# Kernel tuning notes

Hardware: AMD Instinct MI355X
Metric: run time of the kernel (lower is better)

The kernel has to match this reference:

```python
import jax, jax.numpy as jnp
import numpy as np

N = 50000          # nodes
E = 600000         # edges (before self-loops)
IN = 256           # input feature dim
HID = 64           # hidden channels per head
HEADS = 4          # attention heads (hidden layers)
OUT = 64           # output channels (last layer, heads=1)
NEG_SLOPE = 0.2    # PyG GATConv default leaky-relu slope


def setup_inputs() -> dict:
    key = jax.random.key(0)
    ks = jax.random.split(key, 16)
    s = 0.05
    x = jax.random.normal(ks[0], (N, IN), jnp.float32)
    edge_index = jax.random.randint(ks[1], (2, E), 0, N, jnp.int32)
    # layer 0: IN -> HEADS*HID
    W0 = jax.random.normal(ks[2], (IN, HEADS * HID), jnp.float32) * s
    a0s = jax.random.normal(ks[3], (HEADS, HID), jnp.float32) * s
    a0d = jax.random.normal(ks[4], (HEADS, HID), jnp.float32) * s
    b0 = jnp.zeros((HEADS * HID,), jnp.float32)
    # layer 1: HEADS*HID -> HEADS*HID
    W1 = jax.random.normal(ks[5], (HEADS * HID, HEADS * HID), jnp.float32) * s
    a1s = jax.random.normal(ks[6], (HEADS, HID), jnp.float32) * s
    a1d = jax.random.normal(ks[7], (HEADS, HID), jnp.float32) * s
    b1 = jnp.zeros((HEADS * HID,), jnp.float32)
    # layer 2 (output): HEADS*HID -> OUT, heads=1
    W2 = jax.random.normal(ks[8], (HEADS * HID, OUT), jnp.float32) * s
    a2s = jax.random.normal(ks[9], (1, OUT), jnp.float32) * s
    a2d = jax.random.normal(ks[10], (1, OUT), jnp.float32) * s
    b2 = jnp.zeros((OUT,), jnp.float32)
    return dict(x=x, edge_index=edge_index,
                W0=W0, a0s=a0s, a0d=a0d, b0=b0,
                W1=W1, a1s=a1s, a1d=a1d, b1=b1,
                W2=W2, a2s=a2s, a2d=a2d, b2=b2)


def _gat_conv(x, src, dst, deg, W, a_s, a_d, b, heads, out_ch):
    """PyG-style GATConv with self-loops already in (src, dst); mean aggregation."""
    n = x.shape[0]
    h = (x @ W).reshape(n, heads, out_ch)                 # [N, H, C]
    alpha_s = jnp.sum(h * a_s, axis=-1)                   # [N, H]
    alpha_d = jnp.sum(h * a_d, axis=-1)                   # [N, H]
    e = jax.nn.leaky_relu(alpha_s[src] + alpha_d[dst], NEG_SLOPE)  # [Etot, H]
    # segment softmax over incoming edges of each dst node
    m = jax.ops.segment_max(e, dst, num_segments=n)       # [N, H]
    ex = jnp.exp(e - m[dst])
    denom = jax.ops.segment_sum(ex, dst, num_segments=n)  # [N, H]
    alpha = ex / denom[dst]                               # [Etot, H]
    msg = h[src] * alpha[..., None]                       # [Etot, H, C]
    out = jax.ops.segment_sum(msg, dst, num_segments=n)   # [N, H, C]
    out = out / deg[:, None, None]                        # aggr='mean'
    return out.reshape(n, heads * out_ch) + b


def reference(x, edge_index, W0, a0s, a0d, b0, W1, a1s, a1d, b1, W2, a2s, a2d, b2):
    n = x.shape[0]
    # PyG GATConv adds self-loops by default; edge_index constant across layers
    loop = jnp.arange(n, dtype=edge_index.dtype)
    src = jnp.concatenate([edge_index[0], loop])
    dst = jnp.concatenate([edge_index[1], loop])
    deg = jax.ops.segment_sum(jnp.ones(src.shape[0], jnp.float32), dst, num_segments=n)
    h = _gat_conv(x, src, dst, deg, W0, a0s, a0d, b0, HEADS, HID)
    h = jax.nn.relu(h)   # dropout is identity at inference
    h = _gat_conv(h, src, dst, deg, W1, a1s, a1d, b1, HEADS, HID)
    h = jax.nn.relu(h)
    out = _gat_conv(h, src, dst, deg, W2, a2s, a2d, b2, 1, OUT)
    return out
```

## Files before the change

kernel.cpp:

```cpp
#include <hip/hip_runtime.h>
#include <hip/hip_fp16.h>

#define NEG_SLOPE 0.2f

typedef _Float16 f16x8 __attribute__((ext_vector_type(8)));
typedef _Float16 f16x4 __attribute__((ext_vector_type(4)));
typedef float f32x4 __attribute__((ext_vector_type(4)));

__global__ void zero_int_kernel(int* __restrict__ p, int n) {
  int i = blockIdx.x * blockDim.x + threadIdx.x;
  if (i < n) p[i] = 0;
}

__global__ void zero2_float_kernel(float* __restrict__ p1, float* __restrict__ p2,
                                   int n) {
  int i = blockIdx.x * blockDim.x + threadIdx.x;
  if (i < n) { p1[i] = 0.f; p2[i] = 0.f; }
}

__global__ void count_kernel(const int* __restrict__ ei, int E, int N,
                             int* __restrict__ cnt) {
  int e = blockIdx.x * blockDim.x + threadIdx.x;
  int tot = E + N;
  if (e >= tot) return;
  int dst = (e < E) ? ei[E + e] : (e - E);
  atomicAdd(&cnt[dst], 1);
}

__global__ __launch_bounds__(256) void scanA_kernel(const int* __restrict__ cnt,
                                                    int* __restrict__ locex,
                                                    int* __restrict__ blk_sum,
                                                    int N) {
  int t = threadIdx.x;
  int base = blockIdx.x * 1024 + t * 4;
  int a0 = 0, a1 = 0, a2 = 0, a3 = 0;
  if (base + 3 < N) {
    int4 v = *(const int4*)&cnt[base];
    a0 = v.x; a1 = v.y; a2 = v.z; a3 = v.w;
  } else if (base < N) {
    a0 = cnt[base];
    if (base + 1 < N) a1 = cnt[base + 1];
    if (base + 2 < N) a2 = cnt[base + 2];
  }
  int s1 = a0 + a1, s2 = s1 + a2, s3 = s2 + a3;
  int tot = s3;
  int lane = t & 63, wid = t >> 6;
  int ws = tot;
#pragma unroll
  for (int off = 1; off < 64; off <<= 1) {
    int u = __shfl_up(ws, off, 64);
    if (lane >= off) ws += u;
  }
  __shared__ int wsum[4];
  __shared__ int woff[4];
  if (lane == 63) wsum[wid] = ws;
  __syncthreads();
  if (t == 0) {
    int r = 0;
#pragma unroll
    for (int i = 0; i < 4; ++i) { woff[i] = r; r += wsum[i]; }
    blk_sum[blockIdx.x] = r;
  }
  __syncthreads();
  int ex = woff[wid] + (ws - tot);
  int o0 = ex, o1 = ex + a0, o2 = ex + s1, o3 = ex + s2;
  if (base + 3 < N) {
    *(int4*)&locex[base] = make_int4(o0, o1, o2, o3);
  } else if (base < N) {
    locex[base] = o0;
    if (base + 1 < N) locex[base + 1] = o1;
    if (base + 2 < N) locex[base + 2] = o2;
  }
}

__global__ void scanB_kernel(const int* __restrict__ blk_sum,
                             int* __restrict__ blk_off,
                             int* __restrict__ row_ptr, int nb, int N) {
  int t = threadIdx.x;
  int run = 0;
  for (int c = 0; c < nb; c += 64) {
    int idx = c + t;
    int v = (idx < nb) ? blk_sum[idx] : 0;
    int inc = v;
#pragma unroll
    for (int off = 1; off < 64; off <<= 1) {
      int u = __shfl_up(inc, off, 64);
      if (t >= off) inc += u;
    }
    if (idx < nb) blk_off[idx] = run + inc - v;
    run += __shfl(inc, 63, 64);
  }
  if (t == 0) row_ptr[N] = run;
}

__global__ void scanC_kernel(const int* __restrict__ locex,
                             const int* __restrict__ blk_off,
                             int* __restrict__ row_ptr,
                             int* __restrict__ cursor, int N) {
  int i = blockIdx.x * blockDim.x + threadIdx.x;
  if (i >= N) return;
  int v = blk_off[i >> 10] + locex[i];
  row_ptr[i] = v;
  cursor[i] = v;
}

__global__ void fill_kernel(const int* __restrict__ ei, int E, int N,
                            int* __restrict__ cursor, int* __restrict__ col_src) {
  int e = blockIdx.x * blockDim.x + threadIdx.x;
  int tot = E + N;
  if (e >= tot) return;
  int src, dst;
  if (e < E) { src = ei[e]; dst = ei[E + e]; } else { src = e - E; dst = e - E; }
  int pos = atomicAdd(&cursor[dst], 1);
  col_src[pos] = src;
}

template <int BN, int H>
__global__ __launch_bounds__(256) void mfma_gemm(const float* __restrict__ X,
                                                 const float* __restrict__ W,
                                                 __half* __restrict__ Y16,
                                                 const float* __restrict__ aS,
                                                 const float* __restrict__ aD,
                                                 float* __restrict__ as_out,
                                                 float* __restrict__ ad_out,
                                                 int M, int N, int K) {
  constexpr int BM = 128, BK = 32;
  constexpr int LDK = BK + 8;
  constexpr int MI = (BN == 128) ? 4 : 2;
  constexpr int NI = 4;
  constexpr int CK = BN / 8;
  __shared__ _Float16 Ah[BM][LDK];
  __shared__ _Float16 Al[BM][LDK];
  __shared__ _Float16 Bh[BN][LDK];
  __shared__ _Float16 Bl[BN][LDK];
  int tid = threadIdx.x;
  int wave = tid >> 6, lane = tid & 63;
  int quad = lane >> 4, l16 = lane & 15;
  int br = blockIdx.y * BM, bc = blockIdx.x * BN;
  int wm = (BN == 128) ? (wave >> 1) * 64 : wave * 32;
  int wn = (BN == 128) ? (wave & 1) * 64 : 0;
  int bn = tid % BN;
  int bkh = (tid / BN) * CK;

  f32x4 acc[MI][NI] = {};

  for (int k0 = 0; k0 < K; k0 += BK) {
#pragma unroll
    for (int i = 0; i < 4; ++i) {
      int f = tid + i * 256;
      int row = f >> 3;
      int kq = (f & 7) * 4;
      int gm = br + row;
      float4 v = make_float4(0.f, 0.f, 0.f, 0.f);
      if (gm < M) v = *(const float4*)&X[(size_t)gm * K + k0 + kq];
      f16x4 hi, lo;
      hi[0] = (_Float16)v.x; lo[0] = (_Float16)(v.x - (float)hi[0]);
      hi[1] = (_Float16)v.y; lo[1] = (_Float16)(v.y - (float)hi[1]);
      hi[2] = (_Float16)v.z; lo[2] = (_Float16)(v.z - (float)hi[2]);
      hi[3] = (_Float16)v.w; lo[3] = (_Float16)(v.w - (float)hi[3]);
      *(f16x4*)&Ah[row][kq] = hi;
      *(f16x4*)&Al[row][kq] = lo;
    }
    {
      float tmp[CK];
#pragma unroll
      for (int i = 0; i < CK; ++i)
        tmp[i] = W[(size_t)(k0 + bkh + i) * N + bc + bn];
#pragma unroll
      for (int c = 0; c < CK / 8; ++c) {
        f16x8 hi8, lo8;
#pragma unroll
        for (int j = 0; j < 8; ++j) {
          float v = tmp[c * 8 + j];
          _Float16 h = (_Float16)v;
          hi8[j] = h;
          lo8[j] = (_Float16)(v - (float)h);
        }
        *(f16x8*)&Bh[bn][bkh + c * 8] = hi8;
        *(f16x8*)&Bl[bn][bkh + c * 8] = lo8;
      }
    }
    __syncthreads();
    f16x8 fah[MI], fal[MI], fbh[NI], fbl[NI];
#pragma unroll
    for (int mi = 0; mi < MI; ++mi) {
      int row = wm + mi * 16 + l16;
      fah[mi] = *(const f16x8*)&Ah[row][quad * 8];
      fal[mi] = *(const f16x8*)&Al[row][quad * 8];
    }
#pragma unroll
    for (int ni = 0; ni < NI; ++ni) {
      int col = wn + ni * 16 + l16;
      fbh[ni] = *(const f16x8*)&Bh[col][quad * 8];
      fbl[ni] = *(const f16x8*)&Bl[col][quad * 8];
    }
#pragma unroll
    for (int mi = 0; mi < MI; ++mi)
#pragma unroll
      for (int ni = 0; ni < NI; ++ni) {
        acc[mi][ni] = __builtin_amdgcn_mfma_f32_16x16x32_f16(
            fah[mi], fbh[ni], acc[mi][ni], 0, 0, 0);
        acc[mi][ni] = __builtin_amdgcn_mfma_f32_16x16x32_f16(
            fah[mi], fbl[ni], acc[mi][ni], 0, 0, 0);
        acc[mi][ni] = __builtin_amdgcn_mfma_f32_16x16x32_f16(
            fal[mi], fbh[ni], acc[mi][ni], 0, 0, 0);
      }
    __syncthreads();
  }

#pragma unroll
  for (int mi = 0; mi < MI; ++mi) {
#pragma unroll
    for (int r = 0; r < 4; ++r) {
      int grow = br + wm + mi * 16 + quad * 4 + r;
      if (grow >= M) continue;
#pragma unroll
      for (int ni = 0; ni < NI; ++ni) {
        int gcol = bc + wn + ni * 16 + l16;
        Y16[(size_t)grow * N + gcol] = __float2half(acc[mi][ni][r]);
      }
    }
  }

  int head = (bc + wn) >> 6;
  float as_v[NI], ad_v[NI];
#pragma unroll
  for (int ni = 0; ni < NI; ++ni) {
    int c = (wn + ni * 16 + l16) & 63;
    as_v[ni] = aS[head * 64 + c];
    ad_v[ni] = aD[head * 64 + c];
  }
#pragma unroll
  for (int mi = 0; mi < MI; ++mi) {
#pragma unroll
    for (int r = 0; r < 4; ++r) {
      float s = 0.f, d = 0.f;
#pragma unroll
      for (int ni = 0; ni < NI; ++ni) {
        s += acc[mi][ni][r] * as_v[ni];
        d += acc[mi][ni][r] * ad_v[ni];
      }
      s += __shfl_xor(s, 1, 64); d += __shfl_xor(d, 1, 64);
      s += __shfl_xor(s, 2, 64); d += __shfl_xor(d, 2, 64);
      s += __shfl_xor(s, 4, 64); d += __shfl_xor(d, 4, 64);
      s += __shfl_xor(s, 8, 64); d += __shfl_xor(d, 8, 64);
      if (l16 == 0) {
        int grow = br + wm + mi * 16 + quad * 4 + r;
        if (grow < M) {
          atomicAdd(&as_out[(size_t)grow * H + head], s);
          atomicAdd(&ad_out[(size_t)grow * H + head], d);
        }
      }
    }
  }
}

__device__ __forceinline__ void fma_h4(const __half* p, float w, float* facc) {
  union { float2 f2; __half2 h2[2]; } c;
  c.f2 = *(const float2*)p;
  float2 lo = __half22float2(c.h2[0]);
  float2 hi = __half22float2(c.h2[1]);
  facc[0] += lo.x * w; facc[1] += lo.y * w;
  facc[2] += hi.x * w; facc[3] += hi.y * w;
}

template <bool RELU>
__global__ void aggregate4_kernel(const __half* __restrict__ h16,
                                  const float* __restrict__ as_,
                                  const float* __restrict__ ad_,
                                  const int* __restrict__ row_ptr,
                                  const int* __restrict__ col_src,
                                  const float* __restrict__ bias,
                                  float* __restrict__ out, int N) {
  int lane = threadIdx.x & 63;
  int node = (blockIdx.x * blockDim.x + threadIdx.x) >> 6;
  if (node >= N) return;
  int beg = row_ptr[node], end = row_ptr[node + 1];
  int deg = end - beg;
  float inv_deg = 1.f / (float)deg;
  int myhead = lane >> 4;
  float facc[4] = {};
  float4 adv4 = *(const float4*)(ad_ + (size_t)node * 4);
  const __half* hl = h16 + lane * 4;

  if (deg <= 16) {
    int head_w = lane >> 4, e_w = lane & 15;
    float q = 0.f; int s_w = 0;
    if (e_w < deg) {
      s_w = col_src[beg + e_w];
      float4 a4 = *(const float4*)(as_ + (size_t)s_w * 4);
      float av = head_w == 0 ? a4.x : head_w == 1 ? a4.y : head_w == 2 ? a4.z : a4.w;
      float dv = head_w == 0 ? adv4.x : head_w == 1 ? adv4.y : head_w == 2 ? adv4.z : adv4.w;
      float e = av + dv;
      e = (e > 0.f) ? e : NEG_SLOPE * e;
      q = __expf(e);
    }
    float dn = q;
    dn += __shfl_xor(dn, 1, 64);
    dn += __shfl_xor(dn, 2, 64);
    dn += __shfl_xor(dn, 4, 64);
    dn += __shfl_xor(dn, 8, 64);
    float qs = q * (1.f / dn) * inv_deg;
    int base = myhead << 4;
    int i = 0;
    for (; i + 4 <= deg; i += 4) {
      int s0 = __shfl(s_w, base + i + 0, 64); float w0 = __shfl(qs, base + i + 0, 64);
      int s1 = __shfl(s_w, base + i + 1, 64); float w1 = __shfl(qs, base + i + 1, 64);
      int s2 = __shfl(s_w, base + i + 2, 64); float w2 = __shfl(qs, base + i + 2, 64);
      int s3 = __shfl(s_w, base + i + 3, 64); float w3 = __shfl(qs, base + i + 3, 64);
      fma_h4(hl + (size_t)s0 * 256, w0, facc);
      fma_h4(hl + (size_t)s1 * 256, w1, facc);
      fma_h4(hl + (size_t)s2 * 256, w2, facc);
      fma_h4(hl + (size_t)s3 * 256, w3, facc);
    }
    for (; i < deg; ++i) {
      int srcn = __shfl(s_w, base + i, 64);
      float w = __shfl(qs, base + i, 64);
      fma_h4(hl + (size_t)srcn * 256, w, facc);
    }
  } else if (deg <= 64) {
    float p0 = 0.f, p1 = 0.f, p2 = 0.f, p3 = 0.f; int s_w = 0;
    if (lane < deg) {
      s_w = col_src[beg + lane];
      float4 a4 = *(const float4*)(as_ + (size_t)s_w * 4);
      float e0 = a4.x + adv4.x; e0 = e0 > 0.f ? e0 : NEG_SLOPE * e0; p0 = __expf(e0);
      float e1 = a4.y + adv4.y; e1 = e1 > 0.f ? e1 : NEG_SLOPE * e1; p1 = __expf(e1);
      float e2 = a4.z + adv4.z; e2 = e2 > 0.f ? e2 : NEG_SLOPE * e2; p2 = __expf(e2);
      float e3 = a4.w + adv4.w; e3 = e3 > 0.f ? e3 : NEG_SLOPE * e3; p3 = __expf(e3);
    }
    float d0 = p0, d1 = p1, d2 = p2, d3 = p3;
#pragma unroll
    for (int off = 32; off >= 1; off >>= 1) {
      d0 += __shfl_xor(d0, off, 64);
      d1 += __shfl_xor(d1, off, 64);
      d2 += __shfl_xor(d2, off, 64);
      d3 += __shfl_xor(d3, off, 64);
    }
    p0 *= (1.f / d0) * inv_deg;
    p1 *= (1.f / d1) * inv_deg;
    p2 *= (1.f / d2) * inv_deg;
    p3 *= (1.f / d3) * inv_deg;
    int i = 0;
    for (; i + 2 <= deg; i += 2) {
      int s0 = __shfl(s_w, i + 0, 64);
      int s1 = __shfl(s_w, i + 1, 64);
      float a00 = __shfl(p0, i + 0, 64), a01 = __shfl(p1, i + 0, 64);
      float a02 = __shfl(p2, i + 0, 64), a03 = __shfl(p3, i + 0, 64);
      float a10 = __shfl(p0, i + 1, 64), a11 = __shfl(p1, i + 1, 64);
      float a12 = __shfl(p2, i + 1, 64), a13 = __shfl(p3, i + 1, 64);
      float w0 = myhead == 0 ? a00 : myhead == 1 ? a01 : myhead == 2 ? a02 : a03;
      float w1 = myhead == 0 ? a10 : myhead == 1 ? a11 : myhead == 2 ? a12 : a13;
      fma_h4(hl + (size_t)s0 * 256, w0, facc);
      fma_h4(hl + (size_t)s1 * 256, w1, facc);
    }
    for (; i < deg; ++i) {
      int srcn = __shfl(s_w, i, 64);
      float b0 = __shfl(p0, i, 64), b1 = __shfl(p1, i, 64);
      float b2 = __shfl(p2, i, 64), b3 = __shfl(p3, i, 64);
      float w = myhead == 0 ? b0 : myhead == 1 ? b1 : myhead == 2 ? b2 : b3;
      fma_h4(hl + (size_t)srcn * 256, w, facc);
    }
  } else {
    float dn0 = 0.f, dn1 = 0.f, dn2 = 0.f, dn3 = 0.f;
    for (int i = beg + lane; i < end; i += 64) {
      int s = col_src[i];
      float4 a4 = *(const float4*)(as_ + (size_t)s * 4);
      float e0 = a4.x + adv4.x; e0 = e0 > 0.f ? e0 : NEG_SLOPE * e0; dn0 += __expf(e0);
      float e1 = a4.y + adv4.y; e1 = e1 > 0.f ? e1 : NEG_SLOPE * e1; dn1 += __expf(e1);
      float e2 = a4.z + adv4.z; e2 = e2 > 0.f ? e2 : NEG_SLOPE * e2; dn2 += __expf(e2);
      float e3 = a4.w + adv4.w; e3 = e3 > 0.f ? e3 : NEG_SLOPE * e3; dn3 += __expf(e3);
    }
#pragma unroll
    for (int off = 32; off >= 1; off >>= 1) {
      dn0 += __shfl_xor(dn0, off, 64);
      dn1 += __shfl_xor(dn1, off, 64);
      dn2 += __shfl_xor(dn2, off, 64);
      dn3 += __shfl_xor(dn3, off, 64);
    }
    float adm = myhead == 0 ? adv4.x : myhead == 1 ? adv4.y : myhead == 2 ? adv4.z : adv4.w;
    float invdn = 1.f / (myhead == 0 ? dn0 : myhead == 1 ? dn1 : myhead == 2 ? dn2 : dn3);
    invdn *= inv_deg;
    for (int i = beg; i < end; ++i) {
      int s = col_src[i];
      float e = as_[(size_t)s * 4 + myhead] + adm;
      e = (e > 0.f) ? e : NEG_SLOPE * e;
      float w = __expf(e) * invdn;
      fma_h4(hl + (size_t)s * 256, w, facc);
    }
  }

  float* orow = out + (size_t)node * 256 + lane * 4;
#pragma unroll
  for (int p = 0; p < 4; ++p) {
    float v = facc[p] + bias[lane * 4 + p];
    if (RELU) v = fmaxf(v, 0.f);
    orow[p] = v;
  }
}

template <bool RELU>
__global__ void aggregate1_kernel(const __half* __restrict__ h16,
                                  const float* __restrict__ as_,
                                  const float* __restrict__ ad_,
                                  const int* __restrict__ row_ptr,
                                  const int* __restrict__ col_src,
                                  const float* __restrict__ bias,
                                  float* __restrict__ out, int N) {
  int lane = threadIdx.x & 63;
  int node = (blockIdx.x * blockDim.x + threadIdx.x) >> 6;
  if (node >= N) return;
  int beg = row_ptr[node], end = row_ptr[node + 1];
  int deg = end - beg;
  float inv_deg = 1.f / (float)deg;
  float adv = ad_[node];
  const __half* hb = h16 + lane;
  float facc = 0.f;

  if (deg <= 64) {
    float q = 0.f; int s_w = 0;
    if (lane < deg) {
      s_w = col_src[beg + lane];
      float e = as_[s_w] + adv;
      e = (e > 0.f) ? e : NEG_SLOPE * e;
      q = __expf(e);
    }
    float dn = q;
#pragma unroll
    for (int off = 32; off >= 1; off >>= 1) dn += __shfl_xor(dn, off, 64);
    float qs = q * (1.f / dn) * inv_deg;
    int deg8 = (deg + 7) & ~7;
    for (int i = 0; i < deg8; i += 8) {
      int s0 = __shfl(s_w, i + 0, 64); float w0 = __shfl(qs, i + 0, 64);
      int s1 = __shfl(s_w, i + 1, 64); float w1 = __shfl(qs, i + 1, 64);
      int s2 = __shfl(s_w, i + 2, 64); float w2 = __shfl(qs, i + 2, 64);
      int s3 = __shfl(s_w, i + 3, 64); float w3 = __shfl(qs, i + 3, 64);
      int s4 = __shfl(s_w, i + 4, 64); float w4 = __shfl(qs, i + 4, 64);
      int s5 = __shfl(s_w, i + 5, 64); float w5 = __shfl(qs, i + 5, 64);
      int s6 = __shfl(s_w, i + 6, 64); float w6 = __shfl(qs, i + 6, 64);
      int s7 = __shfl(s_w, i + 7, 64); float w7 = __shfl(qs, i + 7, 64);
      float v0 = __half2float(hb[(size_t)s0 * 64]);
      float v1 = __half2float(hb[(size_t)s1 * 64]);
      float v2 = __half2float(hb[(size_t)s2 * 64]);
      float v3 = __half2float(hb[(size_t)s3 * 64]);
      float v4 = __half2float(hb[(size_t)s4 * 64]);
      float v5 = __half2float(hb[(size_t)s5 * 64]);
      float v6 = __half2float(hb[(size_t)s6 * 64]);
      float v7 = __half2float(hb[(size_t)s7 * 64]);
      facc += v0 * w0 + v1 * w1 + v2 * w2 + v3 * w3;
      facc += v4 * w4 + v5 * w5 + v6 * w6 + v7 * w7;
    }
  } else {
    float dn = 0.f;
    for (int i = beg + lane; i < end; i += 64) {
      int s = col_src[i];
      float e = as_[s] + adv;
      e = (e > 0.f) ? e : NEG_SLOPE * e;
      dn += __expf(e);
    }
#pragma unroll
    for (int off = 32; off >= 1; off >>= 1) dn += __shfl_xor(dn, off, 64);
    float scale = (1.f / dn) * inv_deg;
    for (int base = beg; base < end; base += 64) {
      int i2 = base + lane;
      float q2 = 0.f; int s2r = 0;
      if (i2 < end) {
        s2r = col_src[i2];
        float e = as_[s2r] + adv;
        e = (e > 0.f) ? e : NEG_SLOPE * e;
        q2 = __expf(e) * scale;
      }
      int cnt = end - base; if (cnt > 64) cnt = 64;
      for (int j = 0; j < cnt; ++j) {
        int s = __shfl(s2r, j, 64);
        float w = __shfl(q2, j, 64);
        facc += __half2float(hb[(size_t)s * 64]) * w;
      }
    }
  }

  float vout = facc + bias[lane];
  if (RELU) vout = fmaxf(vout, 0.f);
  out[(size_t)node * 64 + lane] = vout;
}

extern "C" void kernel_launch(void* const* d_in, const int* in_sizes, int n_in,
                              void* d_out, int out_size, void* d_ws, size_t ws_size,
                              hipStream_t stream) {
  const float* x   = (const float*)d_in[0];
  const int*   ei  = (const int*)d_in[1];
  const float* W0  = (const float*)d_in[2];
  const float* a0s = (const float*)d_in[3];
  const float* a0d = (const float*)d_in[4];
  const float* b0  = (const float*)d_in[5];
  const float* W1  = (const float*)d_in[6];
  const float* a1s = (const float*)d_in[7];
  const float* a1d = (const float*)d_in[8];
  const float* b1  = (const float*)d_in[9];
  const float* W2  = (const float*)d_in[10];
  const float* a2s = (const float*)d_in[11];
  const float* a2d = (const float*)d_in[12];
  const float* b2  = (const float*)d_in[13];

  const int IN = 256;
  const int N = in_sizes[0] / IN;
  const int E = in_sizes[1] / 2;
  const int Etot = E + N;
  const int nb = (N + 1023) / 1024;

  char* ws = (char*)d_ws;
  size_t off = 0;
  auto alloc = [&](size_t bytes) {
    void* p = ws + off;
    off += (bytes + 255) & ~(size_t)255;
    return p;
  };
  float*  Bbuf    = (float*)alloc((size_t)N * 256 * 4);
  __half* A16     = (__half*)alloc((size_t)N * 256 * 2);
  float*  as_buf  = (float*)alloc((size_t)N * 4 * 4);
  float*  ad_buf  = (float*)alloc((size_t)N * 4 * 4);
  int*    row_ptr = (int*)alloc((size_t)(N + 1) * 4);
  int*    cursor  = (int*)alloc((size_t)N * 4);
  int*    cnt     = (int*)alloc((size_t)N * 4);
  int*    col_src = (int*)alloc((size_t)Etot * 4);
  int*    locex   = (int*)alloc((size_t)N * 4);
  int*    blk_sum = (int*)alloc((size_t)nb * 4);
  int*    blk_off = (int*)alloc((size_t)nb * 4);

  zero_int_kernel<<<(N + 255) / 256, 256, 0, stream>>>(cnt, N);
  count_kernel<<<(Etot + 255) / 256, 256, 0, stream>>>(ei, E, N, cnt);
  scanA_kernel<<<nb, 256, 0, stream>>>(cnt, locex, blk_sum, N);
  scanB_kernel<<<1, 64, 0, stream>>>(blk_sum, blk_off, row_ptr, nb, N);
  scanC_kernel<<<(N + 255) / 256, 256, 0, stream>>>(locex, blk_off, row_ptr, cursor, N);
  fill_kernel<<<(Etot + 255) / 256, 256, 0, stream>>>(ei, E, N, cursor, col_src);

  dim3 g0(256 / 128, (N + 127) / 128);
  dim3 g2(64 / 64, (N + 127) / 128);
  int node_blocks = (N + 3) / 4;
  int zblk4 = (N * 4 + 255) / 256;
  int zblk1 = (N + 255) / 256;

  zero2_float_kernel<<<zblk4, 256, 0, stream>>>(as_buf, ad_buf, N * 4);
  mfma_gemm<128, 4><<<g0, 256, 0, stream>>>(x, W0, A16, a0s, a0d,
                                            as_buf, ad_buf, N, 256, 256);
  aggregate4_kernel<true><<<node_blocks, 256, 0, stream>>>(
      A16, as_buf, ad_buf, row_ptr, col_src, b0, Bbuf, N);

  zero2_float_kernel<<<zblk4, 256, 0, stream>>>(as_buf, ad_buf, N * 4);
  mfma_gemm<128, 4><<<g0, 256, 0, stream>>>(Bbuf, W1, A16, a1s, a1d,
                                            as_buf, ad_buf, N, 256, 256);
  aggregate4_kernel<true><<<node_blocks, 256, 0, stream>>>(
      A16, as_buf, ad_buf, row_ptr, col_src, b1, Bbuf, N);

  zero2_float_kernel<<<zblk1, 256, 0, stream>>>(as_buf, ad_buf, N);
  mfma_gemm<64, 1><<<g2, 256, 0, stream>>>(Bbuf, W2, A16, a2s, a2d,
                                           as_buf, ad_buf, N, 64, 256);
  aggregate1_kernel<false><<<node_blocks, 256, 0, stream>>>(
      A16, as_buf, ad_buf, row_ptr, col_src, b2, (float*)d_out, N);
}
```

Before: 468.4 us.

## Pre-split weights to fp16 and load GEMM fragments directly from global memory

New measurement: 470.5 us. No clear change (+0.5%).

```diff
diff --git a/kernel.cpp b/kernel.cpp
--- a/kernel.cpp
+++ b/kernel.cpp
@@ -4,18 +4,11 @@
 #define NEG_SLOPE 0.2f
 
 typedef _Float16 f16x8 __attribute__((ext_vector_type(8)));
-typedef _Float16 f16x4 __attribute__((ext_vector_type(4)));
 typedef float f32x4 __attribute__((ext_vector_type(4)));
 
 __global__ void zero_int_kernel(int* __restrict__ p, int n) {
   int i = blockIdx.x * blockDim.x + threadIdx.x;
   if (i < n) p[i] = 0;
-}
-
-__global__ void zero2_float_kernel(float* __restrict__ p1, float* __restrict__ p2,
-                                   int n) {
-  int i = blockIdx.x * blockDim.x + threadIdx.x;
-  if (i < n) { p1[i] = 0.f; p2[i] = 0.f; }
 }
 
 __global__ void count_kernel(const int* __restrict__ ei, int E, int N,
@@ -115,84 +108,79 @@
   col_src[pos] = src;
 }
 
-template <int BN, int H>
+__global__ void wsplit_kernel(const float* __restrict__ W,
+                              _Float16* __restrict__ Wth,
+                              _Float16* __restrict__ Wtl, int K, int N) {
+  int idx = blockIdx.x * blockDim.x + threadIdx.x;
+  if (idx >= K * N) return;
+  int n = idx / K, k = idx - n * K;
+  float v = W[(size_t)k * N + n];
+  _Float16 h = (_Float16)v;
+  Wth[idx] = h;
+  Wtl[idx] = (_Float16)(v - (float)h);
+}
+
+template <int BN, int H, int K>
 __global__ __launch_bounds__(256) void mfma_gemm(const float* __restrict__ X,
-                                                 const float* __restrict__ W,
+                                                 const _Float16* __restrict__ Wth,
+                                                 const _Float16* __restrict__ Wtl,
                                                  __half* __restrict__ Y16,
                                                  const float* __restrict__ aS,
                                                  const float* __restrict__ aD,
                                                  float* __restrict__ as_out,
                                                  float* __restrict__ ad_out,
-                                                 int M, int N, int K) {
+                                                 int M, int N) {
   constexpr int BM = 128, BK = 32;
-  constexpr int LDK = BK + 8;
   constexpr int MI = (BN == 128) ? 4 : 2;
   constexpr int NI = 4;
-  constexpr int CK = BN / 8;
-  __shared__ _Float16 Ah[BM][LDK];
-  __shared__ _Float16 Al[BM][LDK];
-  __shared__ _Float16 Bh[BN][LDK];
-  __shared__ _Float16 Bl[BN][LDK];
   int tid = threadIdx.x;
   int wave = tid >> 6, lane = tid & 63;
   int quad = lane >> 4, l16 = lane & 15;
   int br = blockIdx.y * BM, bc = blockIdx.x * BN;
   int wm = (BN == 128) ? (wave >> 1) * 64 : wave * 32;
   int wn = (BN == 128) ? (wave & 1) * 64 : 0;
-  int bn = tid % BN;
-  int bkh = (tid / BN) * CK;
 
   f32x4 acc[MI][NI] = {};
 
+  const float* aptr[MI];
+  bool aval[MI];
+#pragma unroll
+  for (int mi = 0; mi < MI; ++mi) {
+    int grow = br + wm + mi * 16 + l16;
+    aval[mi] = grow < M;
+    aptr[mi] = X + (size_t)(aval[mi] ? grow : 0) * K + quad * 8;
+  }
+  const _Float16* bhp[NI];
+  const _Float16* blp[NI];
+#pragma unroll
+  for (int ni = 0; ni < NI; ++ni) {
+    int col = bc + wn + ni * 16 + l16;
+    bhp[ni] = Wth + (size_t)col * K + quad * 8;
+    blp[ni] = Wtl + (size_t)col * K + quad * 8;
+  }
+
+#pragma unroll 2
   for (int k0 = 0; k0 < K; k0 += BK) {
-#pragma unroll
-    for (int i = 0; i < 4; ++i) {
-      int f = tid + i * 256;
-      int row = f >> 3;
-      int kq = (f & 7) * 4;
-      int gm = br + row;
-      float4 v = make_float4(0.f, 0.f, 0.f, 0.f);
-      if (gm < M) v = *(const float4*)&X[(size_t)gm * K + k0 + kq];
-      f16x4 hi, lo;
-      hi[0] = (_Float16)v.x; lo[0] = (_Float16)(v.x - (float)hi[0]);
-      hi[1] = (_Float16)v.y; lo[1] = (_Float16)(v.y - (float)hi[1]);
-      hi[2] = (_Float16)v.z; lo[2] = (_Float16)(v.z - (float)hi[2]);
-      hi[3] = (_Float16)v.w; lo[3] = (_Float16)(v.w - (float)hi[3]);
-      *(f16x4*)&Ah[row][kq] = hi;
-      *(f16x4*)&Al[row][kq] = lo;
-    }
-    {
-      float tmp[CK];
-#pragma unroll
-      for (int i = 0; i < CK; ++i)
-        tmp[i] = W[(size_t)(k0 + bkh + i) * N + bc + bn];
-#pragma unroll
-      for (int c = 0; c < CK / 8; ++c) {
-        f16x8 hi8, lo8;
-#pragma unroll
-        for (int j = 0; j < 8; ++j) {
-          float v = tmp[c * 8 + j];
-          _Float16 h = (_Float16)v;
-          hi8[j] = h;
-          lo8[j] = (_Float16)(v - (float)h);
-        }
-        *(f16x8*)&Bh[bn][bkh + c * 8] = hi8;
-        *(f16x8*)&Bl[bn][bkh + c * 8] = lo8;
-      }
-    }
-    __syncthreads();
     f16x8 fah[MI], fal[MI], fbh[NI], fbl[NI];
 #pragma unroll
+    for (int ni = 0; ni < NI; ++ni) {
+      fbh[ni] = *(const f16x8*)(bhp[ni] + k0);
+      fbl[ni] = *(const f16x8*)(blp[ni] + k0);
+    }
+#pragma unroll
     for (int mi = 0; mi < MI; ++mi) {
-      int row = wm + mi * 16 + l16;
-      fah[mi] = *(const f16x8*)&Ah[row][quad * 8];
-      fal[mi] = *(const f16x8*)&Al[row][quad * 8];
-    }
-#pragma unroll
-    for (int ni = 0; ni < NI; ++ni) {
-      int col = wn + ni * 16 + l16;
-      fbh[ni] = *(const f16x8*)&Bh[col][quad * 8];
-      fbl[ni] = *(const f16x8*)&Bl[col][quad * 8];
+      float4 v0 = make_float4(0.f, 0.f, 0.f, 0.f), v1 = v0;
+      if (aval[mi]) {
+        v0 = *(const float4*)(aptr[mi] + k0);
+        v1 = *(const float4*)(aptr[mi] + k0 + 4);
+      }
+      float vv[8] = {v0.x, v0.y, v0.z, v0.w, v1.x, v1.y, v1.z, v1.w};
+#pragma unroll
+      for (int j = 0; j < 8; ++j) {
+        _Float16 h = (_Float16)vv[j];
+        fah[mi][j] = h;
+        fal[mi][j] = (_Float16)(vv[j] - (float)h);
+      }
     }
 #pragma unroll
     for (int mi = 0; mi < MI; ++mi)
@@ -205,7 +193,6 @@
         acc[mi][ni] = __builtin_amdgcn_mfma_f32_16x16x32_f16(
             fal[mi], fbh[ni], acc[mi][ni], 0, 0, 0);
       }
-    __syncthreads();
   }
 
 #pragma unroll
@@ -247,8 +234,8 @@
       if (l16 == 0) {
         int grow = br + wm + mi * 16 + quad * 4 + r;
         if (grow < M) {
-          atomicAdd(&as_out[(size_t)grow * H + head], s);
-          atomicAdd(&ad_out[(size_t)grow * H + head], d);
+          as_out[(size_t)grow * H + head] = s;
+          ad_out[(size_t)grow * H + head] = d;
         }
       }
     }
@@ -514,17 +501,19 @@
     off += (bytes + 255) & ~(size_t)255;
     return p;
   };
-  float*  Bbuf    = (float*)alloc((size_t)N * 256 * 4);
-  __half* A16     = (__half*)alloc((size_t)N * 256 * 2);
-  float*  as_buf  = (float*)alloc((size_t)N * 4 * 4);
-  float*  ad_buf  = (float*)alloc((size_t)N * 4 * 4);
-  int*    row_ptr = (int*)alloc((size_t)(N + 1) * 4);
-  int*    cursor  = (int*)alloc((size_t)N * 4);
-  int*    cnt     = (int*)alloc((size_t)N * 4);
-  int*    col_src = (int*)alloc((size_t)Etot * 4);
-  int*    locex   = (int*)alloc((size_t)N * 4);
-  int*    blk_sum = (int*)alloc((size_t)nb * 4);
-  int*    blk_off = (int*)alloc((size_t)nb * 4);
+  float*    Bbuf    = (float*)alloc((size_t)N * 256 * 4);
+  __half*   A16     = (__half*)alloc((size_t)N * 256 * 2);
+  float*    as_buf  = (float*)alloc((size_t)N * 4 * 4);
+  float*    ad_buf  = (float*)alloc((size_t)N * 4 * 4);
+  int*      row_ptr = (int*)alloc((size_t)(N + 1) * 4);
+  int*      cursor  = (int*)alloc((size_t)N * 4);
+  int*      cnt     = (int*)alloc((size_t)N * 4);
+  int*      col_src = (int*)alloc((size_t)Etot * 4);
+  int*      locex   = (int*)alloc((size_t)N * 4);
+  int*      blk_sum = (int*)alloc((size_t)nb * 4);
+  int*      blk_off = (int*)alloc((size_t)nb * 4);
+  _Float16* Wth     = (_Float16*)alloc((size_t)256 * 256 * 2);
+  _Float16* Wtl     = (_Float16*)alloc((size_t)256 * 256 * 2);
 
   zero_int_kernel<<<(N + 255) / 256, 256, 0, stream>>>(cnt, N);
   count_kernel<<<(Etot + 255) / 256, 256, 0, stream>>>(ei, E, N, cnt);
@@ -536,24 +525,22 @@
   dim3 g0(256 / 128, (N + 127) / 128);
   dim3 g2(64 / 64, (N + 127) / 128);
   int node_blocks = (N + 3) / 4;
-  int zblk4 = (N * 4 + 255) / 256;
-  int zblk1 = (N + 255) / 256;
-
-  zero2_float_kernel<<<zblk4, 256, 0, stream>>>(as_buf, ad_buf, N * 4);
-  mfma_gemm<128, 4><<<g0, 256, 0, stream>>>(x, W0, A16, a0s, a0d,
-                                            as_buf, ad_buf, N, 256, 256);
+
+  wsplit_kernel<<<(256 * 256 + 255) / 256, 256, 0, stream>>>(W0, Wth, Wtl, 256, 256);
+  mfma_gemm<128, 4, 256><<<g0, 256, 0, stream>>>(x, Wth, Wtl, A16, a0s, a0d,
+                                                 as_buf, ad_buf, N, 256);
   aggregate4_kernel<true><<<node_blocks, 256, 0, stream>>>(
       A16, as_buf, ad_buf, row_ptr, col_src, b0, Bbuf, N);
 
-  zero2_float_kernel<<<zblk4, 256, 0, stream>>>(as_buf, ad_buf, N * 4);
-  mfma_gemm<128, 4><<<g0, 256, 0, stream>>>(Bbuf, W1, A16, a1s, a1d,
-                                            as_buf, ad_buf, N, 256, 256);
+  wsplit_kernel<<<(256 * 256 + 255) / 256, 256, 0, stream>>>(W1, Wth, Wtl, 256, 256);
+  mfma_gemm<128, 4, 256><<<g0, 256, 0, stream>>>(Bbuf, Wth, Wtl, A16, a1s, a1d,
+                                                 as_buf, ad_buf, N, 256);
   aggregate4_kernel<true><<<node_blocks, 256, 0, stream>>>(
       A16, as_buf, ad_buf, row_ptr, col_src, b1, Bbuf, N);
 
-  zero2_float_kernel<<<zblk1, 256, 0, stream>>>(as_buf, ad_buf, N);
-  mfma_gemm<64, 1><<<g2, 256, 0, stream>>>(Bbuf, W2, A16, a2s, a2d,
-                                           as_buf, ad_buf, N, 64, 256);
+  wsplit_kernel<<<(256 * 64 + 255) / 256, 256, 0, stream>>>(W2, Wth, Wtl, 256, 64);
+  mfma_gemm<64, 1, 256><<<g2, 256, 0, stream>>>(Bbuf, Wth, Wtl, A16, a2s, a2d,
+                                                as_buf, ad_buf, N, 64);
   aggregate1_kernel<false><<<node_blocks, 256, 0, stream>>>(
       A16, as_buf, ad_buf, row_ptr, col_src, b2, (float*)d_out, N);
 }
```
